# Performance work log

Measured on AMD Instinct MI355X. Metric: run time of the kernel, lower is better.

## Reference

```python
import jax, jax.numpy as jnp
import numpy as np
import math

N = 4096
D = 256


def _xavier(key, shape):
    fan_in, fan_out = shape[0], shape[1]
    std = math.sqrt(2.0 / (fan_in + fan_out))
    return jax.random.normal(key, shape, dtype=jnp.float32) * std


def setup_inputs() -> dict:
    key = jax.random.key(0)
    ks = jax.random.split(key, 12)
    return {
        "cur": jax.random.normal(ks[0], (N, D), dtype=jnp.float32),
        "pre": jax.random.normal(ks[1], (N, D), dtype=jnp.float32),
        # SpatialHyperedge params
        "r_proj_s": _xavier(ks[2], (D, D)),
        "incidence_s": _xavier(ks[3], (N, N - 1)),
        # TemporalHyperedge params
        "r_proj_t": _xavier(ks[4], (D, D)),
        "incidence_t": _xavier(ks[5], (N, N)),
        # HHNodeMP params
        "node_proj": _xavier(ks[6], (D, D)),
        "spa_edge_proj": _xavier(ks[7], (D, D)),
        "tmp_edge_proj": _xavier(ks[8], (D, D)),
        "theta_w": _xavier(ks[9], (D, D)),
        "theta_b": jnp.zeros((D,), dtype=jnp.float32),
    }


def _scatter_slave(vals):
    """Place [N, N-1] per-row slave values into a zero-diagonal [N, N] matrix.
    Row i's k-th slave is column k if k < i else k+1 (all j != i in order)."""
    n = vals.shape[0]
    k = jnp.arange(n - 1)[None, :]
    cols = k + (k >= jnp.arange(n)[:, None])  # [N, N-1] column indices
    rows = jnp.broadcast_to(jnp.arange(n)[:, None], (n, n - 1))
    return jnp.zeros((n, n), dtype=vals.dtype).at[rows.reshape(-1), cols.reshape(-1)].set(vals.reshape(-1))


def _fro(x):
    return jnp.sqrt(jnp.sum(x * x))


def reference(cur, pre, r_proj_s, incidence_s, r_proj_t, incidence_t,
              node_proj, spa_edge_proj, tmp_edge_proj, theta_w, theta_b):
    n, d = cur.shape
    inv_sqrt_d = 1.0 / math.sqrt(d)

    # ---- SpatialHyperedge ----
    Xd = jax.lax.stop_gradient(cur)
    master_s = Xd @ r_proj_s                                   # [N, D]
    M_s_full = _scatter_slave(incidence_s)                     # [N, N], zero diag
    neigh_recon_s = M_s_full @ Xd                              # == bmm over gathered slaves
    spatial_loss = (_fro(master_s - neigh_recon_s) * 0.2
                    + jnp.sum(jnp.abs(incidence_s))
                    + 0.001 * _fro(incidence_s))
    # clamp(min=0) then zero-out entries not strictly > 0  => relu-like
    clipped_s = jnp.where(incidence_s > 0.0, incidence_s, 0.0)
    incidence_all = _scatter_slave(clipped_s) + jnp.eye(n, dtype=cur.dtype)

    # ---- TemporalHyperedge ----
    cur_d = jax.lax.stop_gradient(cur)
    pre_d = jax.lax.stop_gradient(pre)
    master_t = cur_d @ r_proj_t
    neigh_recon_t = incidence_t @ pre_d
    temporal_loss = (_fro(master_t - neigh_recon_t) * 0.2
                     + jnp.sum(jnp.abs(incidence_t))
                     + 0.001 * _fro(incidence_t))
    incidence_t_clipped = jnp.maximum(incidence_t, 0.0)

    # ---- SpatialHyperedgeMP ----
    spa_edge_fea = incidence_all @ cur
    spa_deg = jnp.sum(incidence_all, axis=1, keepdims=True)
    spa_emb = spa_edge_fea / spa_deg                           # [N, D]

    # ---- TemporalHyperedgeMP ----
    tmp_edge_fea = incidence_t_clipped @ pre + cur
    tmp_deg = jnp.sum(incidence_t_clipped, axis=1, keepdims=True) + 1.0
    tmp_emb = tmp_edge_fea / tmp_deg                           # [N, D]

    # ---- HHNodeMP ----
    node_fea = cur @ node_proj
    spa_fea = spa_emb @ spa_edge_proj
    tmp_fea = tmp_emb @ tmp_edge_proj
    spa_attn = jnp.sum(spa_fea * node_fea, axis=1, keepdims=True) * inv_sqrt_d
    tmp_attn = jnp.sum(tmp_fea * node_fea, axis=1, keepdims=True) * inv_sqrt_d
    val = spa_attn * spa_fea + tmp_attn * tmp_fea
    node_emb = jax.nn.relu(val @ theta_w.T + theta_b)          # dropout = identity (eval)

    return node_emb, temporal_loss + spatial_loss
```

## Files before the change

### kernel.cpp

```cpp
#include <hip/hip_runtime.h>
#include <hip/hip_bf16.h>
#include <math.h>

#define NN 4096
#define DD 256

typedef __bf16 bf16x8 __attribute__((ext_vector_type(8)));
typedef short  short8 __attribute__((ext_vector_type(8)));
typedef float  f32x4  __attribute__((ext_vector_type(4)));

#define MFMA16(a, b, c) __builtin_amdgcn_mfma_f32_16x16x32_bf16((a), (b), (c), 0, 0, 0)

__device__ inline bf16x8 brelu(bf16x8 a) {
    short8 s = __builtin_bit_cast(short8, a);
    s = s & ~(s >> 15);
    return __builtin_bit_cast(bf16x8, s);
}

__device__ inline float wave_red(float v) {
#pragma unroll
    for (int o = 32; o > 0; o >>= 1) v += __shfl_down(v, o, 64);
    return v;
}

__device__ inline unsigned short bfbits(float f) {
    return __builtin_bit_cast(unsigned short, (__bf16)f);
}

#define GLL16(g, l) __builtin_amdgcn_global_load_lds( \
    (const __attribute__((address_space(1))) void*)(g), \
    (__attribute__((address_space(3))) void*)(l), 16, 0, 0)

__global__ __launch_bounds__(256) void k_pre(
    const float* __restrict__ cur, const float* __restrict__ pre,
    const float* __restrict__ r_proj_s, const float* __restrict__ inc_s,
    const float* __restrict__ r_proj_t, const float* __restrict__ inc_t,
    const float* __restrict__ node_pj, const float* __restrict__ spa_pj,
    const float* __restrict__ tmp_pj, const float* __restrict__ theta_w,
    __bf16* __restrict__ Mt, __bf16* __restrict__ Ms,
    __bf16* __restrict__ cur_bf, __bf16* __restrict__ curT, __bf16* __restrict__ preT,
    __bf16* __restrict__ pTs, __bf16* __restrict__ pTt, __bf16* __restrict__ pTn,
    __bf16* __restrict__ pTspa, __bf16* __restrict__ pTtmp, __bf16* __restrict__ thetaBf,
    float* __restrict__ rsT, float* __restrict__ rsS,
    float* __restrict__ pAbsT, float* __restrict__ pSqT,
    float* __restrict__ pAbsS, float* __restrict__ pSqS)
{
    __shared__ __align__(16) char sm[9280];
    const int bx = blockIdx.x, t = threadIdx.x;

    if (bx < 8192) {
        float (*red)[4] = (float(*)[4])(sm + 8192 + 16);
        float rs = 0.f, as = 0.f, qs = 0.f;
        const int w = t >> 6, lane = t & 63;
        if (bx < 4096) {
            const int i = bx;
            const float4* src = (const float4*)(inc_t + (size_t)i * NN);
            ushort4* dst = (ushort4*)(Mt + (size_t)i * NN);
#pragma unroll
            for (int e = 0; e < 4; ++e) {
                const int f = t + 256 * e;
                float4 v = src[f];
                float x[4] = {v.x, v.y, v.z, v.w};
                unsigned short o[4];
#pragma unroll
                for (int j = 0; j < 4; ++j) {
                    float fv = x[j];
                    as += fabsf(fv); qs += fv * fv; rs += fmaxf(fv, 0.f);
                    o[j] = bfbits(fv);
                }
                dst[f] = make_ushort4(o[0], o[1], o[2], o[3]);
            }
            rs = wave_red(rs); as = wave_red(as); qs = wave_red(qs);
            if (lane == 0) { red[0][w] = rs; red[1][w] = as; red[2][w] = qs; }
            __syncthreads();
            if (t == 0) {
                rsT[i]   = red[0][0] + red[0][1] + red[0][2] + red[0][3];
                pAbsT[i] = red[1][0] + red[1][1] + red[1][2] + red[1][3];
                pSqT[i]  = red[2][0] + red[2][1] + red[2][2] + red[2][3];
            }
        } else {
            const int i = bx - 4096;
            unsigned short* row = (unsigned short*)sm;
            const float* srow = inc_s + (size_t)i * (NN - 1);
#pragma unroll
            for (int e = 0; e < 4; ++e) {
                const int f = t + 256 * e;
                float x[4] = {0.f, 0.f, 0.f, 0.f};
                if (f < 1023) __builtin_memcpy(x, srow + 4 * f, 16);
                else          __builtin_memcpy(x, srow + 4092, 12);
#pragma unroll
                for (int j = 0; j < 4; ++j) {
                    const int k = 4 * f + j;
                    float fv = x[j];
                    as += fabsf(fv); qs += fv * fv; rs += fmaxf(fv, 0.f);
                    if (k < NN - 1) row[k + (k >= i)] = bfbits(fv);
                }
            }
            if (t == 0) row[i] = 0;
            __syncthreads();
            uint4* dOut = (uint4*)(Ms + (size_t)i * NN);
            const uint4* sIn = (const uint4*)row;
            dOut[t] = sIn[t];
            dOut[t + 256] = sIn[t + 256];
            rs = wave_red(rs); as = wave_red(as); qs = wave_red(qs);
            if (lane == 0) { red[0][w] = rs; red[1][w] = as; red[2][w] = qs; }
            __syncthreads();
            if (t == 0) {
                rsS[i]   = red[0][0] + red[0][1] + red[0][2] + red[0][3];
                pAbsS[i] = red[1][0] + red[1][1] + red[1][2] + red[1][3];
                pSqS[i]  = red[2][0] + red[2][1] + red[2][2] + red[2][3];
            }
        }
    } else if (bx < 8704) {
        const int idx = bx - 8192;
        const int z = idx >> 8, yt = (idx >> 6) & 3, xt = idx & 63;
        const int i0 = xt * 64, d0 = yt * 64;
        const float* src = z ? pre : cur;
        __bf16* dstT = z ? preT : curT;
        unsigned short (*tile)[72] = (unsigned short(*)[72])sm;
        const int r = t >> 2, c4 = (t & 3) * 16;
        const float* srow = src + (size_t)(i0 + r) * DD + d0 + c4;
        alignas(16) unsigned short loc[16];
#pragma unroll
        for (int e = 0; e < 4; ++e) {
            float4 v = ((const float4*)srow)[e];
            loc[e * 4 + 0] = bfbits(v.x); loc[e * 4 + 1] = bfbits(v.y);
            loc[e * 4 + 2] = bfbits(v.z); loc[e * 4 + 3] = bfbits(v.w);
        }
#pragma unroll
        for (int e = 0; e < 16; ++e) tile[r][c4 + e] = loc[e];
        if (z == 0) {
            __bf16* drow = cur_bf + (size_t)(i0 + r) * DD + d0 + c4;
            *(uint4*)drow = *(uint4*)&loc[0];
            *(uint4*)(drow + 8) = *(uint4*)&loc[8];
        }
        __syncthreads();
        alignas(16) unsigned short o[16];
#pragma unroll
        for (int e = 0; e < 16; ++e) o[e] = tile[c4 + e][r];
        __bf16* trow = dstT + (size_t)(d0 + r) * NN + i0 + c4;
        *(uint4*)trow = *(uint4*)&o[0];
        *(uint4*)(trow + 8) = *(uint4*)&o[8];
    } else {
        const int idx = bx - 8704;
        const int m = idx >> 4, tt = idx & 15;
        const int k0 = (tt >> 2) * 64, n0 = (tt & 3) * 64;
        const int r = t >> 2, c4 = (t & 3) * 16;
        const float* src = m == 0 ? r_proj_s : m == 1 ? r_proj_t : m == 2 ? node_pj
                         : m == 3 ? spa_pj : m == 4 ? tmp_pj : theta_w;
        __bf16* dst = m == 0 ? pTs : m == 1 ? pTt : m == 2 ? pTn
                    : m == 3 ? pTspa : m == 4 ? pTtmp : thetaBf;
        const float* srow = src + (size_t)(k0 + r) * DD + n0 + c4;
        alignas(16) unsigned short loc[16];
#pragma unroll
        for (int e = 0; e < 4; ++e) {
            float4 v = ((const float4*)srow)[e];
            loc[e * 4 + 0] = bfbits(v.x); loc[e * 4 + 1] = bfbits(v.y);
            loc[e * 4 + 2] = bfbits(v.z); loc[e * 4 + 3] = bfbits(v.w);
        }
        if (m < 5) {
            unsigned short (*tile)[72] = (unsigned short(*)[72])sm;
#pragma unroll
            for (int e = 0; e < 16; ++e) tile[r][c4 + e] = loc[e];
            __syncthreads();
            alignas(16) unsigned short o[16];
#pragma unroll
            for (int e = 0; e < 16; ++e) o[e] = tile[c4 + e][r];
            __bf16* trow = dst + (size_t)(n0 + r) * DD + k0 + c4;
            *(uint4*)trow = *(uint4*)&o[0];
            *(uint4*)(trow + 8) = *(uint4*)&o[8];
        } else {
            __bf16* drow = dst + (size_t)(k0 + r) * DD + n0 + c4;
            *(uint4*)drow = *(uint4*)&loc[0];
            *(uint4*)(drow + 8) = *(uint4*)&loc[8];
        }
    }
}

__global__ __launch_bounds__(256) void k_big(const __bf16* __restrict__ Mt, const __bf16* __restrict__ Ms,
                                             const __bf16* __restrict__ preT, const __bf16* __restrict__ curT,
                                             const float* __restrict__ negMt, const float* __restrict__ negMs,
                                             const float* __restrict__ cur,
                                             float* __restrict__ feaT, float* __restrict__ feaS,
                                             float* __restrict__ pDiff) {
    const int z = blockIdx.z;
    const __bf16* A  = z ? Ms : Mt;
    const __bf16* BT = z ? curT : preT;
    const float* negM = z ? negMs : negMt;
    float* fea = z ? feaS : feaT;
    const int n0 = blockIdx.x * 64, m0 = blockIdx.y * 64;
    __shared__ __align__(16) char smA[2 * 8192];
    __shared__ __align__(16) char smB[2 * 8192];
    __shared__ float sred[4];
    const int t = threadIdx.x, w = t >> 6, lane = t & 63, quad = lane >> 4, l16 = lane & 15;
    const int wr = w >> 1, wc = w & 1;

    const int lr = lane >> 3, lk = lane & 7;
    const int kswz = (lk ^ lr) << 3;
    const __bf16* gA0 = A + (size_t)(m0 + w * 16 + lr) * NN + kswz;
    const __bf16* gA1 = A + (size_t)(m0 + w * 16 + 8 + lr) * NN + kswz;
    const __bf16* gB0 = BT + (size_t)(n0 + w * 16 + lr) * NN + kswz;
    const __bf16* gB1 = BT + (size_t)(n0 + w * 16 + 8 + lr) * NN + kswz;
    char* lA0 = smA + (w * 16) * 128;
    char* lA1 = smA + (w * 16 + 8) * 128;
    char* lB0 = smB + (w * 16) * 128;
    char* lB1 = smB + (w * 16 + 8) * 128;

#define STAGE(bo, kt) do { const size_t ko = (size_t)(kt) * 64; \
        GLL16(gA0 + ko, lA0 + (bo)); GLL16(gA1 + ko, lA1 + (bo)); \
        GLL16(gB0 + ko, lB0 + (bo)); GLL16(gB1 + ko, lB1 + (bo)); } while (0)

    f32x4 accR[2][2], accL[2][2];
#pragma unroll
    for (int i = 0; i < 2; ++i)
#pragma unroll
        for (int j = 0; j < 2; ++j) { accR[i][j] = (f32x4)0.f; accL[i][j] = (f32x4)0.f; }

    const int s7 = l16 & 7;
    const int aoff0 = (wr * 32 + l16) * 128;
    const int boff0 = (wc * 32 + l16) * 128;

    STAGE(0, 0);
    __syncthreads();

#pragma unroll 2
    for (int kt = 0; kt < 64; ++kt) {
        const int cb = (kt & 1) * 8192;
        if (kt < 63) STAGE(cb ^ 8192, kt + 1);
        const char* Ab = smA + cb;
        const char* Bb = smB + cb;
#pragma unroll
        for (int ks = 0; ks < 2; ++ks) {
            const int slot = ((ks * 4 + quad) ^ s7) << 4;
            bf16x8 a0 = *(const bf16x8*)(Ab + aoff0 + slot);
            bf16x8 a1 = *(const bf16x8*)(Ab + aoff0 + 2048 + slot);
            bf16x8 b0 = *(const bf16x8*)(Bb + boff0 + slot);
            bf16x8 b1 = *(const bf16x8*)(Bb + boff0 + 2048 + slot);
            bf16x8 a0r = brelu(a0), a1r = brelu(a1);
            accR[0][0] = MFMA16(a0, b0, accR[0][0]);
            accR[0][1] = MFMA16(a0, b1, accR[0][1]);
            accR[1][0] = MFMA16(a1, b0, accR[1][0]);
            accR[1][1] = MFMA16(a1, b1, accR[1][1]);
            accL[0][0] = MFMA16(a0r, b0, accL[0][0]);
            accL[0][1] = MFMA16(a0r, b1, accL[0][1]);
            accL[1][0] = MFMA16(a1r, b0, accL[1][0]);
            accL[1][1] = MFMA16(a1r, b1, accL[1][1]);
        }
        __syncthreads();
    }
#undef STAGE

    float sumd = 0.f;
#pragma unroll
    for (int mi = 0; mi < 2; ++mi)
#pragma unroll
        for (int ni = 0; ni < 2; ++ni)
#pragma unroll
            for (int r = 0; r < 4; ++r) {
                int gr = m0 + wr * 32 + mi * 16 + quad * 4 + r;
                int gc = n0 + wc * 32 + ni * 16 + l16;
                size_t idx = (size_t)gr * DD + gc;
                float diff = accR[mi][ni][r] + negM[idx];
                sumd += diff * diff;
                fea[idx] = accL[mi][ni][r] + cur[idx];
            }
    sumd = wave_red(sumd);
    if (lane == 0) sred[w] = sumd;
    __syncthreads();
    if (t == 0)
        pDiff[z * 256 + blockIdx.y * 4 + blockIdx.x] = sred[0] + sred[1] + sred[2] + sred[3];
}

__device__ inline void mfma_step0(const __bf16 (*As)[72], const __bf16 (*Bs)[72],
                                  int wr, int wc, int quad, int l16, f32x4 (&acc)[2][2]) {
#pragma unroll
    for (int ks = 0; ks < 2; ++ks) {
        const int kc = ks * 32 + quad * 8;
        bf16x8 a0 = *(const bf16x8*)&As[wr * 32 + l16][kc];
        bf16x8 a1 = *(const bf16x8*)&As[wr * 32 + 16 + l16][kc];
        bf16x8 b0 = *(const bf16x8*)&Bs[wc * 32 + l16][kc];
        bf16x8 b1 = *(const bf16x8*)&Bs[wc * 32 + 16 + l16][kc];
        acc[0][0] = MFMA16(a0, b0, acc[0][0]);
        acc[0][1] = MFMA16(a0, b1, acc[0][1]);
        acc[1][0] = MFMA16(a1, b0, acc[1][0]);
        acc[1][1] = MFMA16(a1, b1, acc[1][1]);
    }
}

__global__ __launch_bounds__(256) void k_small3(const __bf16* __restrict__ cur_bf,
                                                const __bf16* __restrict__ pTs, const __bf16* __restrict__ pTt,
                                                const __bf16* __restrict__ pTn,
                                                float* __restrict__ negMs, float* __restrict__ negMt,
                                                float* __restrict__ nodeFea) {
    const int z = blockIdx.z;
    const __bf16* BT = z == 0 ? pTs : (z == 1 ? pTt : pTn);
    const int n0 = blockIdx.x * 64, m0 = blockIdx.y * 64;
    __shared__ __bf16 As[64][72], Bs[64][72];
    f32x4 acc[2][2];
#pragma unroll
    for (int i = 0; i < 2; ++i)
#pragma unroll
        for (int j = 0; j < 2; ++j) acc[i][j] = (f32x4)0.f;
    const int t = threadIdx.x, w = t >> 6, lane = t & 63, quad = lane >> 4, l16 = lane & 15;
    const int wr = w >> 1, wc = w & 1;
    const int sr = t >> 2, sc = (t & 3) * 16;
    const __bf16* gA = cur_bf + (size_t)(m0 + sr) * DD + sc;
    const __bf16* gB = BT + (size_t)(n0 + sr) * DD + sc;
    for (int kt = 0; kt < DD / 64; ++kt) {
        uint4 av0 = *(const uint4*)(gA);
        uint4 av1 = *(const uint4*)(gA + 8);
        uint4 bv0 = *(const uint4*)(gB);
        uint4 bv1 = *(const uint4*)(gB + 8);
        __syncthreads();
        *(uint4*)&As[sr][sc] = av0; *(uint4*)&As[sr][sc + 8] = av1;
        *(uint4*)&Bs[sr][sc] = bv0; *(uint4*)&Bs[sr][sc + 8] = bv1;
        __syncthreads();
        mfma_step0(As, Bs, wr, wc, quad, l16, acc);
        gA += 64; gB += 64;
    }
#pragma unroll
    for (int mi = 0; mi < 2; ++mi)
#pragma unroll
        for (int ni = 0; ni < 2; ++ni)
#pragma unroll
            for (int r = 0; r < 4; ++r) {
                int gr = m0 + wr * 32 + mi * 16 + quad * 4 + r;
                int gc = n0 + wc * 32 + ni * 16 + l16;
                size_t o = (size_t)gr * DD + gc;
                float v = acc[mi][ni][r];
                if (z == 0) negMs[o] = -v;
                else if (z == 1) negMt[o] = -v;
                else nodeFea[o] = v;
            }
}

__global__ __launch_bounds__(256) void k_fea(const float* __restrict__ feaS, const float* __restrict__ feaT,
                                             const float* __restrict__ rsS, const float* __restrict__ rsT,
                                             const __bf16* __restrict__ pTspa, const __bf16* __restrict__ pTtmp,
                                             float* __restrict__ spaF, float* __restrict__ tmpF) {
    const int z = blockIdx.z;
    const float* fea = z ? feaT : feaS;
    const float* rs = z ? rsT : rsS;
    const __bf16* BT = z ? pTtmp : pTspa;
    float* outF = z ? tmpF : spaF;
    const int n0 = blockIdx.x * 64, m0 = blockIdx.y * 64;
    __shared__ __bf16 As[64][72], Bs[64][72];
    f32x4 acc[2][2];
#pragma unroll
    for (int i = 0; i < 2; ++i)
#pragma unroll
        for (int j = 0; j < 2; ++j) acc[i][j] = (f32x4)0.f;
    const int t = threadIdx.x, w = t >> 6, lane = t & 63, quad = lane >> 4, l16 = lane & 15;
    const int wr = w >> 1, wc = w & 1;
    const int sr = t >> 2, sc = (t & 3) * 16;
    const float inv = 1.f / (rs[m0 + sr] + 1.f);
    const float* gA = fea + (size_t)(m0 + sr) * DD + sc;
    const __bf16* gB = BT + (size_t)(n0 + sr) * DD + sc;
    for (int kt = 0; kt < DD / 64; ++kt) {
        __bf16 tmp[16];
#pragma unroll
        for (int e4 = 0; e4 < 4; ++e4) {
            float4 v = ((const float4*)gA)[e4];
            tmp[e4 * 4 + 0] = (__bf16)(v.x * inv);
            tmp[e4 * 4 + 1] = (__bf16)(v.y * inv);
            tmp[e4 * 4 + 2] = (__bf16)(v.z * inv);
            tmp[e4 * 4 + 3] = (__bf16)(v.w * inv);
        }
        uint4 bv0 = *(const uint4*)(gB);
        uint4 bv1 = *(const uint4*)(gB + 8);
        __syncthreads();
        *(uint4*)&As[sr][sc] = *(uint4*)&tmp[0]; *(uint4*)&As[sr][sc + 8] = *(uint4*)&tmp[8];
        *(uint4*)&Bs[sr][sc] = bv0; *(uint4*)&Bs[sr][sc + 8] = bv1;
        __syncthreads();
        mfma_step0(As, Bs, wr, wc, quad, l16, acc);
        gA += 64; gB += 64;
    }
#pragma unroll
    for (int mi = 0; mi < 2; ++mi)
#pragma unroll
        for (int ni = 0; ni < 2; ++ni)
#pragma unroll
            for (int r = 0; r < 4; ++r) {
                int gr = m0 + wr * 32 + mi * 16 + quad * 4 + r;
                int gc = n0 + wc * 32 + ni * 16 + l16;
                outF[(size_t)gr * DD + gc] = acc[mi][ni][r];
            }
}

__global__ __launch_bounds__(256) void k_attn(const float* __restrict__ spaF, const float* __restrict__ tmpF,
                                              const float* __restrict__ nodeF,
                                              float* __restrict__ spaA, float* __restrict__ tmpA) {
    const int t = threadIdx.x, w = t >> 6, lane = t & 63;
    const int i = blockIdx.x * 4 + w;
    const float4* sf = (const float4*)(spaF + (size_t)i * DD);
    const float4* tf = (const float4*)(tmpF + (size_t)i * DD);
    const float4* nf = (const float4*)(nodeF + (size_t)i * DD);
    float4 s = sf[lane], p = tf[lane], n = nf[lane];
    float ds = s.x * n.x + s.y * n.y + s.z * n.z + s.w * n.w;
    float dt = p.x * n.x + p.y * n.y + p.z * n.z + p.w * n.w;
    ds = wave_red(ds); dt = wave_red(dt);
    if (lane == 0) { spaA[i] = ds * 0.0625f; tmpA[i] = dt * 0.0625f; }
}

__global__ __launch_bounds__(256) void k_final(const float* __restrict__ spaF, const float* __restrict__ tmpF,
                                               const float* __restrict__ spaA, const float* __restrict__ tmpA,
                                               const __bf16* __restrict__ thetaBf, const float* __restrict__ thetaB,
                                               float* __restrict__ out) {
    const int n0 = blockIdx.x * 64, m0 = blockIdx.y * 64;
    __shared__ __bf16 As[64][72], Bs[64][72];
    f32x4 acc[2][2];
#pragma unroll
    for (int i = 0; i < 2; ++i)
#pragma unroll
        for (int j = 0; j < 2; ++j) acc[i][j] = (f32x4)0.f;
    const int t = threadIdx.x, w = t >> 6, lane = t & 63, quad = lane >> 4, l16 = lane & 15;
    const int wr = w >> 1, wc = w & 1;
    const int sr = t >> 2, sc = (t & 3) * 16;
    const float sa = spaA[m0 + sr], ta = tmpA[m0 + sr];
    const float* gS = spaF + (size_t)(m0 + sr) * DD + sc;
    const float* gT = tmpF + (size_t)(m0 + sr) * DD + sc;
    const __bf16* gB = thetaBf + (size_t)(n0 + sr) * DD + sc;
    for (int kt = 0; kt < DD / 64; ++kt) {
        __bf16 tmp[16];
#pragma unroll
        for (int e4 = 0; e4 < 4; ++e4) {
            float4 vs = ((const float4*)gS)[e4];
            float4 vt = ((const float4*)gT)[e4];
            tmp[e4 * 4 + 0] = (__bf16)(sa * vs.x + ta * vt.x);
            tmp[e4 * 4 + 1] = (__bf16)(sa * vs.y + ta * vt.y);
            tmp[e4 * 4 + 2] = (__bf16)(sa * vs.z + ta * vt.z);
            tmp[e4 * 4 + 3] = (__bf16)(sa * vs.w + ta * vt.w);
        }
        uint4 bv0 = *(const uint4*)(gB);
        uint4 bv1 = *(const uint4*)(gB + 8);
        __syncthreads();
        *(uint4*)&As[sr][sc] = *(uint4*)&tmp[0]; *(uint4*)&As[sr][sc + 8] = *(uint4*)&tmp[8];
        *(uint4*)&Bs[sr][sc] = bv0; *(uint4*)&Bs[sr][sc + 8] = bv1;
        __syncthreads();
        mfma_step0(As, Bs, wr, wc, quad, l16, acc);
        gS += 64; gT += 64; gB += 64;
    }
#pragma unroll
    for (int mi = 0; mi < 2; ++mi)
#pragma unroll
        for (int ni = 0; ni < 2; ++ni)
#pragma unroll
            for (int r = 0; r < 4; ++r) {
                int gr = m0 + wr * 32 + mi * 16 + quad * 4 + r;
                int gc = n0 + wc * 32 + ni * 16 + l16;
                float v = acc[mi][ni][r] + thetaB[gc];
                out[(size_t)gr * DD + gc] = fmaxf(v, 0.f);
            }
}

__global__ __launch_bounds__(256) void k_loss(const float* __restrict__ pAbsT, const float* __restrict__ pSqT,
                                              const float* __restrict__ pAbsS, const float* __restrict__ pSqS,
                                              const float* __restrict__ pDiff,
                                              float* __restrict__ out) {
    const int t = threadIdx.x;
    float aT = 0.f, qT = 0.f, aS = 0.f, qS = 0.f;
#pragma unroll
    for (int j = 0; j < 16; ++j) {
        const int i = t + 256 * j;
        aT += pAbsT[i]; qT += pSqT[i]; aS += pAbsS[i]; qS += pSqS[i];
    }
    float dT = pDiff[t], dS = pDiff[256 + t];
    aT = wave_red(aT); qT = wave_red(qT); aS = wave_red(aS); qS = wave_red(qS);
    dT = wave_red(dT); dS = wave_red(dS);
    __shared__ float red[6][4];
    const int w = t >> 6, lane = t & 63;
    if (lane == 0) { red[0][w] = aT; red[1][w] = qT; red[2][w] = aS; red[3][w] = qS; red[4][w] = dT; red[5][w] = dS; }
    __syncthreads();
    if (t == 0) {
        float s[6];
#pragma unroll
        for (int k = 0; k < 6; ++k) s[k] = red[k][0] + red[k][1] + red[k][2] + red[k][3];
        float l = s[0] + 0.001f * sqrtf(s[1]) + 0.2f * sqrtf(s[4])
                + s[2] + 0.001f * sqrtf(s[3]) + 0.2f * sqrtf(s[5]);
        out[(size_t)NN * DD] = l;
    }
}

extern "C" void kernel_launch(void* const* d_in, const int* in_sizes, int n_in,
                              void* d_out, int out_size, void* d_ws, size_t ws_size,
                              hipStream_t stream) {
    (void)in_sizes; (void)n_in; (void)out_size; (void)ws_size;
    const float* cur      = (const float*)d_in[0];
    const float* pre      = (const float*)d_in[1];
    const float* r_proj_s = (const float*)d_in[2];
    const float* inc_s    = (const float*)d_in[3];
    const float* r_proj_t = (const float*)d_in[4];
    const float* inc_t    = (const float*)d_in[5];
    const float* node_pj  = (const float*)d_in[6];
    const float* spa_pj   = (const float*)d_in[7];
    const float* tmp_pj   = (const float*)d_in[8];
    const float* theta_w  = (const float*)d_in[9];
    const float* theta_b  = (const float*)d_in[10];
    float* out = (float*)d_out;

    char* p = (char*)d_ws;
    auto alloc = [&](size_t bytes) -> void* {
        void* r = (void*)p;
        p += (bytes + 255) & ~(size_t)255;
        return r;
    };
    __bf16* Mt      = (__bf16*)alloc((size_t)NN * NN * 2);
    __bf16* Ms      = (__bf16*)alloc((size_t)NN * NN * 2);
    __bf16* cur_bf  = (__bf16*)alloc((size_t)NN * DD * 2);
    __bf16* curT    = (__bf16*)alloc((size_t)NN * DD * 2);
    __bf16* preT    = (__bf16*)alloc((size_t)NN * DD * 2);
    __bf16* pTs     = (__bf16*)alloc((size_t)DD * DD * 2);
    __bf16* pTt     = (__bf16*)alloc((size_t)DD * DD * 2);
    __bf16* pTn     = (__bf16*)alloc((size_t)DD * DD * 2);
    __bf16* pTspa   = (__bf16*)alloc((size_t)DD * DD * 2);
    __bf16* pTtmp   = (__bf16*)alloc((size_t)DD * DD * 2);
    __bf16* thetaBf = (__bf16*)alloc((size_t)DD * DD * 2);
    float* negMs    = (float*)alloc((size_t)NN * DD * 4);
    float* negMt    = (float*)alloc((size_t)NN * DD * 4);
    float* nodeFea  = (float*)alloc((size_t)NN * DD * 4);
    float* feaS     = (float*)alloc((size_t)NN * DD * 4);
    float* feaT     = (float*)alloc((size_t)NN * DD * 4);
    float* spaF     = (float*)alloc((size_t)NN * DD * 4);
    float* tmpF     = (float*)alloc((size_t)NN * DD * 4);
    float* rsS      = (float*)alloc((size_t)NN * 4);
    float* rsT      = (float*)alloc((size_t)NN * 4);
    float* spaA     = (float*)alloc((size_t)NN * 4);
    float* tmpA     = (float*)alloc((size_t)NN * 4);
    float* pAbsT    = (float*)alloc((size_t)NN * 4);
    float* pSqT     = (float*)alloc((size_t)NN * 4);
    float* pAbsS    = (float*)alloc((size_t)NN * 4);
    float* pSqS     = (float*)alloc((size_t)NN * 4);
    float* pDiff    = (float*)alloc(512 * 4);

    k_pre<<<8800, 256, 0, stream>>>(cur, pre, r_proj_s, inc_s, r_proj_t, inc_t,
                                    node_pj, spa_pj, tmp_pj, theta_w,
                                    Mt, Ms, cur_bf, curT, preT,
                                    pTs, pTt, pTn, pTspa, pTtmp, thetaBf,
                                    rsT, rsS, pAbsT, pSqT, pAbsS, pSqS);
    k_small3<<<dim3(4, 64, 3), 256, 0, stream>>>(cur_bf, pTs, pTt, pTn, negMs, negMt, nodeFea);
    k_big<<<dim3(4, 64, 2), 256, 0, stream>>>(Mt, Ms, preT, curT, negMt, negMs, cur, feaT, feaS, pDiff);
    k_fea<<<dim3(4, 64, 2), 256, 0, stream>>>(feaS, feaT, rsS, rsT, pTspa, pTtmp, spaF, tmpF);
    k_attn<<<NN / 4, 256, 0, stream>>>(spaF, tmpF, nodeFea, spaA, tmpA);
    k_final<<<dim3(4, 64), 256, 0, stream>>>(spaF, tmpF, spaA, tmpA, thetaBf, theta_b, out);
    k_loss<<<1, 256, 0, stream>>>(pAbsT, pSqT, pAbsS, pSqS, pDiff, out);
}
```

Before: 272.4 us.

## Split preprocessing kernel and retile big GEMM to 32-row tiles with register staging

Splits the monolithic preprocessing kernel into separate temporal/spatial incidence conversion kernels and a misc transpose kernel. The spatial conversion now writes the shifted bf16 row directly from registers instead of through shared memory. The big GEMM halves the M tile to 32 rows, doubling grid size, and replaces the double-buffered async global_load_lds pipeline with single-buffered register loads plus two barriers per k-step. Partial-diff buffer doubles and the loss kernel sums the extra partials. This gains occupancy/parallelism but loses load/compute overlap and B reuse.

New measurement: 271.5 us. No clear change (-0.3%).

```diff
diff --git a/kernel.cpp b/kernel.cpp
--- a/kernel.cpp
+++ b/kernel.cpp
@@ -27,98 +27,104 @@
     return __builtin_bit_cast(unsigned short, (__bf16)f);
 }
 
-#define GLL16(g, l) __builtin_amdgcn_global_load_lds( \
-    (const __attribute__((address_space(1))) void*)(g), \
-    (__attribute__((address_space(3))) void*)(l), 16, 0, 0)
-
-__global__ __launch_bounds__(256) void k_pre(
+__global__ __launch_bounds__(256) void k_conv_t(const float* __restrict__ inc,
+                                                __bf16* __restrict__ Mbf,
+                                                float* __restrict__ rowsum,
+                                                float* __restrict__ pAbs, float* __restrict__ pSq) {
+    const int i = blockIdx.x, t = threadIdx.x;
+    const float4* src = (const float4*)(inc + (size_t)i * NN);
+    ushort4* dst = (ushort4*)(Mbf + (size_t)i * NN);
+    float rs = 0.f, as = 0.f, qs = 0.f;
+#pragma unroll
+    for (int e = 0; e < 4; ++e) {
+        const int f = t + 256 * e;
+        float4 v = src[f];
+        float x[4] = {v.x, v.y, v.z, v.w};
+        unsigned short o[4];
+#pragma unroll
+        for (int j = 0; j < 4; ++j) {
+            float fv = x[j];
+            as += fabsf(fv); qs += fv * fv; rs += fmaxf(fv, 0.f);
+            o[j] = bfbits(fv);
+        }
+        dst[f] = make_ushort4(o[0], o[1], o[2], o[3]);
+    }
+    __shared__ float red[3][4];
+    const int w = t >> 6, lane = t & 63;
+    rs = wave_red(rs); as = wave_red(as); qs = wave_red(qs);
+    if (lane == 0) { red[0][w] = rs; red[1][w] = as; red[2][w] = qs; }
+    __syncthreads();
+    if (t == 0) {
+        rowsum[i] = red[0][0] + red[0][1] + red[0][2] + red[0][3];
+        pAbs[i]   = red[1][0] + red[1][1] + red[1][2] + red[1][3];
+        pSq[i]    = red[2][0] + red[2][1] + red[2][2] + red[2][3];
+    }
+}
+
+__global__ __launch_bounds__(256) void k_conv_s(const float* __restrict__ inc,
+                                                __bf16* __restrict__ Mbf,
+                                                float* __restrict__ rowsum,
+                                                float* __restrict__ pAbs, float* __restrict__ pSq) {
+    const int i = blockIdx.x, t = threadIdx.x;
+    const float* srow = inc + (size_t)i * (NN - 1);
+    float xs[16];
+    if (t < 255) __builtin_memcpy(xs, srow + 16 * t, 64);
+    else { __builtin_memcpy(xs, srow + 16 * t, 60); xs[15] = 0.f; }
+    float rs = 0.f, as = 0.f, qs = 0.f;
+#pragma unroll
+    for (int e = 0; e < 16; ++e) {
+        float fv = xs[e];
+        as += fabsf(fv); qs += fv * fv; rs += fmaxf(fv, 0.f);
+    }
+    const int base = 16 * t;
+    alignas(16) __bf16 o[16];
+    if (i >= base + 16) {
+#pragma unroll
+        for (int e = 0; e < 16; ++e) o[e] = (__bf16)xs[e];
+    } else if (i < base) {
+        float ys[16];
+        __builtin_memcpy(ys, srow + base - 1, 64);
+#pragma unroll
+        for (int e = 0; e < 16; ++e) o[e] = (__bf16)ys[e];
+    } else {
+#pragma unroll
+        for (int e = 0; e < 16; ++e) {
+            const int j = base + e;
+            o[e] = (j == i) ? (__bf16)0.f : (__bf16)srow[j - (j > i)];
+        }
+    }
+    __bf16* drow = Mbf + (size_t)i * NN + base;
+    *(uint4*)drow = *(uint4*)&o[0];
+    *(uint4*)(drow + 8) = *(uint4*)&o[8];
+    __shared__ float red[3][4];
+    const int w = t >> 6, lane = t & 63;
+    rs = wave_red(rs); as = wave_red(as); qs = wave_red(qs);
+    if (lane == 0) { red[0][w] = rs; red[1][w] = as; red[2][w] = qs; }
+    __syncthreads();
+    if (t == 0) {
+        rowsum[i] = red[0][0] + red[0][1] + red[0][2] + red[0][3];
+        pAbs[i]   = red[1][0] + red[1][1] + red[1][2] + red[1][3];
+        pSq[i]    = red[2][0] + red[2][1] + red[2][2] + red[2][3];
+    }
+}
+
+__global__ __launch_bounds__(256) void k_misc(
     const float* __restrict__ cur, const float* __restrict__ pre,
-    const float* __restrict__ r_proj_s, const float* __restrict__ inc_s,
-    const float* __restrict__ r_proj_t, const float* __restrict__ inc_t,
+    const float* __restrict__ r_proj_s, const float* __restrict__ r_proj_t,
     const float* __restrict__ node_pj, const float* __restrict__ spa_pj,
     const float* __restrict__ tmp_pj, const float* __restrict__ theta_w,
-    __bf16* __restrict__ Mt, __bf16* __restrict__ Ms,
     __bf16* __restrict__ cur_bf, __bf16* __restrict__ curT, __bf16* __restrict__ preT,
     __bf16* __restrict__ pTs, __bf16* __restrict__ pTt, __bf16* __restrict__ pTn,
-    __bf16* __restrict__ pTspa, __bf16* __restrict__ pTtmp, __bf16* __restrict__ thetaBf,
-    float* __restrict__ rsT, float* __restrict__ rsS,
-    float* __restrict__ pAbsT, float* __restrict__ pSqT,
-    float* __restrict__ pAbsS, float* __restrict__ pSqS)
+    __bf16* __restrict__ pTspa, __bf16* __restrict__ pTtmp, __bf16* __restrict__ thetaBf)
 {
-    __shared__ __align__(16) char sm[9280];
+    __shared__ unsigned short tile[64][72];
     const int bx = blockIdx.x, t = threadIdx.x;
-
-    if (bx < 8192) {
-        float (*red)[4] = (float(*)[4])(sm + 8192 + 16);
-        float rs = 0.f, as = 0.f, qs = 0.f;
-        const int w = t >> 6, lane = t & 63;
-        if (bx < 4096) {
-            const int i = bx;
-            const float4* src = (const float4*)(inc_t + (size_t)i * NN);
-            ushort4* dst = (ushort4*)(Mt + (size_t)i * NN);
-#pragma unroll
-            for (int e = 0; e < 4; ++e) {
-                const int f = t + 256 * e;
-                float4 v = src[f];
-                float x[4] = {v.x, v.y, v.z, v.w};
-                unsigned short o[4];
-#pragma unroll
-                for (int j = 0; j < 4; ++j) {
-                    float fv = x[j];
-                    as += fabsf(fv); qs += fv * fv; rs += fmaxf(fv, 0.f);
-                    o[j] = bfbits(fv);
-                }
-                dst[f] = make_ushort4(o[0], o[1], o[2], o[3]);
-            }
-            rs = wave_red(rs); as = wave_red(as); qs = wave_red(qs);
-            if (lane == 0) { red[0][w] = rs; red[1][w] = as; red[2][w] = qs; }
-            __syncthreads();
-            if (t == 0) {
-                rsT[i]   = red[0][0] + red[0][1] + red[0][2] + red[0][3];
-                pAbsT[i] = red[1][0] + red[1][1] + red[1][2] + red[1][3];
-                pSqT[i]  = red[2][0] + red[2][1] + red[2][2] + red[2][3];
-            }
-        } else {
-            const int i = bx - 4096;
-            unsigned short* row = (unsigned short*)sm;
-            const float* srow = inc_s + (size_t)i * (NN - 1);
-#pragma unroll
-            for (int e = 0; e < 4; ++e) {
-                const int f = t + 256 * e;
-                float x[4] = {0.f, 0.f, 0.f, 0.f};
-                if (f < 1023) __builtin_memcpy(x, srow + 4 * f, 16);
-                else          __builtin_memcpy(x, srow + 4092, 12);
-#pragma unroll
-                for (int j = 0; j < 4; ++j) {
-                    const int k = 4 * f + j;
-                    float fv = x[j];
-                    as += fabsf(fv); qs += fv * fv; rs += fmaxf(fv, 0.f);
-                    if (k < NN - 1) row[k + (k >= i)] = bfbits(fv);
-                }
-            }
-            if (t == 0) row[i] = 0;
-            __syncthreads();
-            uint4* dOut = (uint4*)(Ms + (size_t)i * NN);
-            const uint4* sIn = (const uint4*)row;
-            dOut[t] = sIn[t];
-            dOut[t + 256] = sIn[t + 256];
-            rs = wave_red(rs); as = wave_red(as); qs = wave_red(qs);
-            if (lane == 0) { red[0][w] = rs; red[1][w] = as; red[2][w] = qs; }
-            __syncthreads();
-            if (t == 0) {
-                rsS[i]   = red[0][0] + red[0][1] + red[0][2] + red[0][3];
-                pAbsS[i] = red[1][0] + red[1][1] + red[1][2] + red[1][3];
-                pSqS[i]  = red[2][0] + red[2][1] + red[2][2] + red[2][3];
-            }
-        }
-    } else if (bx < 8704) {
-        const int idx = bx - 8192;
-        const int z = idx >> 8, yt = (idx >> 6) & 3, xt = idx & 63;
+    const int r = t >> 2, c4 = (t & 3) * 16;
+    if (bx < 512) {
+        const int z = bx >> 8, yt = (bx >> 6) & 3, xt = bx & 63;
         const int i0 = xt * 64, d0 = yt * 64;
         const float* src = z ? pre : cur;
         __bf16* dstT = z ? preT : curT;
-        unsigned short (*tile)[72] = (unsigned short(*)[72])sm;
-        const int r = t >> 2, c4 = (t & 3) * 16;
         const float* srow = src + (size_t)(i0 + r) * DD + d0 + c4;
         alignas(16) unsigned short loc[16];
 #pragma unroll
@@ -142,10 +148,9 @@
         *(uint4*)trow = *(uint4*)&o[0];
         *(uint4*)(trow + 8) = *(uint4*)&o[8];
     } else {
-        const int idx = bx - 8704;
+        const int idx = bx - 512;
         const int m = idx >> 4, tt = idx & 15;
         const int k0 = (tt >> 2) * 64, n0 = (tt & 3) * 64;
-        const int r = t >> 2, c4 = (t & 3) * 16;
         const float* src = m == 0 ? r_proj_s : m == 1 ? r_proj_t : m == 2 ? node_pj
                          : m == 3 ? spa_pj : m == 4 ? tmp_pj : theta_w;
         __bf16* dst = m == 0 ? pTs : m == 1 ? pTt : m == 2 ? pTn
@@ -159,7 +164,6 @@
             loc[e * 4 + 2] = bfbits(v.z); loc[e * 4 + 3] = bfbits(v.w);
         }
         if (m < 5) {
-            unsigned short (*tile)[72] = (unsigned short(*)[72])sm;
 #pragma unroll
             for (int e = 0; e < 16; ++e) tile[r][c4 + e] = loc[e];
             __syncthreads();
@@ -188,87 +192,70 @@
     const __bf16* BT = z ? curT : preT;
     const float* negM = z ? negMs : negMt;
     float* fea = z ? feaS : feaT;
-    const int n0 = blockIdx.x * 64, m0 = blockIdx.y * 64;
-    __shared__ __align__(16) char smA[2 * 8192];
-    __shared__ __align__(16) char smB[2 * 8192];
+    const int n0 = blockIdx.x * 64, m0 = blockIdx.y * 32;
+    __shared__ __align__(16) __bf16 smA[32 * 64];
+    __shared__ __align__(16) __bf16 smB[64 * 64];
     __shared__ float sred[4];
     const int t = threadIdx.x, w = t >> 6, lane = t & 63, quad = lane >> 4, l16 = lane & 15;
     const int wr = w >> 1, wc = w & 1;
 
-    const int lr = lane >> 3, lk = lane & 7;
-    const int kswz = (lk ^ lr) << 3;
-    const __bf16* gA0 = A + (size_t)(m0 + w * 16 + lr) * NN + kswz;
-    const __bf16* gA1 = A + (size_t)(m0 + w * 16 + 8 + lr) * NN + kswz;
-    const __bf16* gB0 = BT + (size_t)(n0 + w * 16 + lr) * NN + kswz;
-    const __bf16* gB1 = BT + (size_t)(n0 + w * 16 + 8 + lr) * NN + kswz;
-    char* lA0 = smA + (w * 16) * 128;
-    char* lA1 = smA + (w * 16 + 8) * 128;
-    char* lB0 = smB + (w * 16) * 128;
-    char* lB1 = smB + (w * 16 + 8) * 128;
-
-#define STAGE(bo, kt) do { const size_t ko = (size_t)(kt) * 64; \
-        GLL16(gA0 + ko, lA0 + (bo)); GLL16(gA1 + ko, lA1 + (bo)); \
-        GLL16(gB0 + ko, lB0 + (bo)); GLL16(gB1 + ko, lB1 + (bo)); } while (0)
-
-    f32x4 accR[2][2], accL[2][2];
-#pragma unroll
-    for (int i = 0; i < 2; ++i)
-#pragma unroll
-        for (int j = 0; j < 2; ++j) { accR[i][j] = (f32x4)0.f; accL[i][j] = (f32x4)0.f; }
+    const int srow = t >> 3, sc = t & 7;
+    const int gsc = (sc ^ (srow & 7)) << 3;
+    const __bf16* gA  = A  + (size_t)(m0 + srow) * NN + gsc;
+    const __bf16* gB0 = BT + (size_t)(n0 + srow) * NN + gsc;
+    const __bf16* gB1 = BT + (size_t)(n0 + srow + 32) * NN + gsc;
+    __bf16* lA  = smA + srow * 64 + sc * 8;
+    __bf16* lB0 = smB + srow * 64 + sc * 8;
+    __bf16* lB1 = smB + (srow + 32) * 64 + sc * 8;
+
+    f32x4 accR[2], accL[2];
+#pragma unroll
+    for (int nf = 0; nf < 2; ++nf) { accR[nf] = (f32x4)0.f; accL[nf] = (f32x4)0.f; }
 
     const int s7 = l16 & 7;
-    const int aoff0 = (wr * 32 + l16) * 128;
-    const int boff0 = (wc * 32 + l16) * 128;
-
-    STAGE(0, 0);
-    __syncthreads();
-
-#pragma unroll 2
+    const __bf16* arow  = smA + (wr * 16 + l16) * 64;
+    const __bf16* brow0 = smB + (wc * 32 + l16) * 64;
+    const __bf16* brow1 = smB + (wc * 32 + 16 + l16) * 64;
+
     for (int kt = 0; kt < 64; ++kt) {
-        const int cb = (kt & 1) * 8192;
-        if (kt < 63) STAGE(cb ^ 8192, kt + 1);
-        const char* Ab = smA + cb;
-        const char* Bb = smB + cb;
+        uint4 va  = *(const uint4*)(gA);
+        uint4 vb0 = *(const uint4*)(gB0);
+        uint4 vb1 = *(const uint4*)(gB1);
+        gA += 64; gB0 += 64; gB1 += 64;
+        __syncthreads();
+        *(uint4*)lA = va; *(uint4*)lB0 = vb0; *(uint4*)lB1 = vb1;
+        __syncthreads();
 #pragma unroll
         for (int ks = 0; ks < 2; ++ks) {
-            const int slot = ((ks * 4 + quad) ^ s7) << 4;
-            bf16x8 a0 = *(const bf16x8*)(Ab + aoff0 + slot);
-            bf16x8 a1 = *(const bf16x8*)(Ab + aoff0 + 2048 + slot);
-            bf16x8 b0 = *(const bf16x8*)(Bb + boff0 + slot);
-            bf16x8 b1 = *(const bf16x8*)(Bb + boff0 + 2048 + slot);
-            bf16x8 a0r = brelu(a0), a1r = brelu(a1);
-            accR[0][0] = MFMA16(a0, b0, accR[0][0]);
-            accR[0][1] = MFMA16(a0, b1, accR[0][1]);
-            accR[1][0] = MFMA16(a1, b0, accR[1][0]);
-            accR[1][1] = MFMA16(a1, b1, accR[1][1]);
-            accL[0][0] = MFMA16(a0r, b0, accL[0][0]);
-            accL[0][1] = MFMA16(a0r, b1, accL[0][1]);
-            accL[1][0] = MFMA16(a1r, b0, accL[1][0]);
-            accL[1][1] = MFMA16(a1r, b1, accL[1][1]);
-        }
-        __syncthreads();
-    }
-#undef STAGE
+            const int so = ((ks * 4 + quad) ^ s7) << 3;
+            bf16x8 a  = *(const bf16x8*)(arow + so);
+            bf16x8 b0 = *(const bf16x8*)(brow0 + so);
+            bf16x8 b1 = *(const bf16x8*)(brow1 + so);
+            bf16x8 ar = brelu(a);
+            accR[0] = MFMA16(a, b0, accR[0]);
+            accR[1] = MFMA16(a, b1, accR[1]);
+            accL[0] = MFMA16(ar, b0, accL[0]);
+            accL[1] = MFMA16(ar, b1, accL[1]);
+        }
+    }
 
     float sumd = 0.f;
 #pragma unroll
-    for (int mi = 0; mi < 2; ++mi)
-#pragma unroll
-        for (int ni = 0; ni < 2; ++ni)
-#pragma unroll
-            for (int r = 0; r < 4; ++r) {
-                int gr = m0 + wr * 32 + mi * 16 + quad * 4 + r;
-                int gc = n0 + wc * 32 + ni * 16 + l16;
-                size_t idx = (size_t)gr * DD + gc;
-                float diff = accR[mi][ni][r] + negM[idx];
-                sumd += diff * diff;
-                fea[idx] = accL[mi][ni][r] + cur[idx];
-            }
+    for (int nf = 0; nf < 2; ++nf)
+#pragma unroll
+        for (int r = 0; r < 4; ++r) {
+            int gr = m0 + wr * 16 + quad * 4 + r;
+            int gc = n0 + wc * 32 + nf * 16 + l16;
+            size_t idx = (size_t)gr * DD + gc;
+            float diff = accR[nf][r] + negM[idx];
+            sumd += diff * diff;
+            fea[idx] = accL[nf][r] + cur[idx];
+        }
     sumd = wave_red(sumd);
     if (lane == 0) sred[w] = sumd;
     __syncthreads();
     if (t == 0)
-        pDiff[z * 256 + blockIdx.y * 4 + blockIdx.x] = sred[0] + sred[1] + sred[2] + sred[3];
+        pDiff[z * 512 + blockIdx.y * 4 + blockIdx.x] = sred[0] + sred[1] + sred[2] + sred[3];
 }
 
 __device__ inline void mfma_step0(const __bf16 (*As)[72], const __bf16 (*Bs)[72],
@@ -464,7 +451,8 @@
         const int i = t + 256 * j;
         aT += pAbsT[i]; qT += pSqT[i]; aS += pAbsS[i]; qS += pSqS[i];
     }
-    float dT = pDiff[t], dS = pDiff[256 + t];
+    float dT = pDiff[t] + pDiff[256 + t];
+    float dS = pDiff[512 + t] + pDiff[768 + t];
     aT = wave_red(aT); qT = wave_red(qT); aS = wave_red(aS); qS = wave_red(qS);
     dT = wave_red(dT); dS = wave_red(dS);
     __shared__ float red[6][4];
@@ -530,15 +518,14 @@
     float* pSqT     = (float*)alloc((size_t)NN * 4);
     float* pAbsS    = (float*)alloc((size_t)NN * 4);
     float* pSqS     = (float*)alloc((size_t)NN * 4);
-    float* pDiff    = (float*)alloc(512 * 4);
-
-    k_pre<<<8800, 256, 0, stream>>>(cur, pre, r_proj_s, inc_s, r_proj_t, inc_t,
-                                    node_pj, spa_pj, tmp_pj, theta_w,
-                                    Mt, Ms, cur_bf, curT, preT,
-                                    pTs, pTt, pTn, pTspa, pTtmp, thetaBf,
-                                    rsT, rsS, pAbsT, pSqT, pAbsS, pSqS);
+    float* pDiff    = (float*)alloc(1024 * 4);
+
+    k_conv_t<<<NN, 256, 0, stream>>>(inc_t, Mt, rsT, pAbsT, pSqT);
+    k_conv_s<<<NN, 256, 0, stream>>>(inc_s, Ms, rsS, pAbsS, pSqS);
+    k_misc<<<608, 256, 0, stream>>>(cur, pre, r_proj_s, r_proj_t, node_pj, spa_pj, tmp_pj, theta_w,
+                                    cur_bf, curT, preT, pTs, pTt, pTn, pTspa, pTtmp, thetaBf);
     k_small3<<<dim3(4, 64, 3), 256, 0, stream>>>(cur_bf, pTs, pTt, pTn, negMs, negMt, nodeFea);
-    k_big<<<dim3(4, 64, 2), 256, 0, stream>>>(Mt, Ms, preT, curT, negMt, negMs, cur, feaT, feaS, pDiff);
+    k_big<<<dim3(4, 128, 2), 256, 0, stream>>>(Mt, Ms, preT, curT, negMt, negMs, cur, feaT, feaS, pDiff);
     k_fea<<<dim3(4, 64, 2), 256, 0, stream>>>(feaS, feaT, rsS, rsT, pTspa, pTtmp, spaF, tmpF);
     k_attn<<<NN / 4, 256, 0, stream>>>(spaF, tmpF, nodeFea, spaA, tmpA);
     k_final<<<dim3(4, 64), 256, 0, stream>>>(spaF, tmpF, spaA, tmpA, thetaBf, theta_b, out);
```
